# Kernel optimization log

Measured on AMD Instinct MI355X. Metric: run time of the kernel, lower is better.

## Reference

```python
import jax, jax.numpy as jnp
import numpy as np
from jax import lax

B, KLEN, KDIM, QDIM, ADIM, VDIM = 32, 2000, 512, 512, 512, 512
CONV_CH, CONV_K = 10, 201

def setup_inputs() -> dict:
    key = jax.random.key(0)
    ks = jax.random.split(key, 16)
    s = lambda fan: 1.0 / np.sqrt(fan)
    return {
        "key": jax.random.normal(ks[0], (B, KLEN, KDIM), jnp.float32),
        "value": jax.random.normal(ks[1], (B, KLEN, VDIM), jnp.float32),
        "query": jax.random.normal(ks[2], (B, 1, QDIM), jnp.float32),
        "aw_prev": jnp.zeros((B, 1, KLEN), jnp.float32),
        "mask": jnp.ones((B, 1, KLEN), jnp.int32),
        # parameters (torch nn.Linear: y = x @ W.T + b, W is [out,in])
        "Wk": jax.random.uniform(ks[3], (ADIM, KDIM), jnp.float32, -s(KDIM), s(KDIM)),
        "bk": jax.random.uniform(ks[4], (ADIM,), jnp.float32, -s(KDIM), s(KDIM)),
        "Wq": jax.random.uniform(ks[5], (ADIM, QDIM), jnp.float32, -s(QDIM), s(QDIM)),
        "conv_w": jax.random.uniform(ks[6], (CONV_CH, 1, CONV_K), jnp.float32, -s(CONV_K), s(CONV_K)),
        "Wconv": jax.random.uniform(ks[7], (ADIM, CONV_CH), jnp.float32, -s(CONV_CH), s(CONV_CH)),
        "v": jax.random.uniform(ks[8], (ADIM,), jnp.float32, -s(ADIM), s(ADIM)),
    }

def reference(key, value, query, aw_prev, mask, Wk, bk, Wq, conv_w, Wconv, v):
    # location-aware attention, qlen == 1, sharpening_factor == 1, no dropout (eval)
    kproj = jnp.einsum('bkd,ad->bka', key, Wk) + bk              # [B, klen, adim]
    qproj = jnp.einsum('bqd,ad->bqa', query, Wq)                 # [B, 1, adim]
    # conv over previous attention weights: 1D 'same' conv, 1 -> CONV_CH channels
    conv_feat = lax.conv_general_dilated(
        aw_prev, conv_w, window_strides=(1,), padding='SAME',
        dimension_numbers=('NCH', 'OIH', 'NCH'))                 # [B, C, klen]
    conv_proj = jnp.einsum('bck,ac->bka', conv_feat, Wconv)      # [B, klen, adim]
    # additive score: v^T tanh(Wk k + Wq q + Wc f)
    tmp = jnp.tanh(kproj[:, None] + qproj[:, :, None] + conv_proj[:, None])  # [B,1,klen,adim]
    e = jnp.einsum('bqka,a->bqk', tmp, v)                        # [B, 1, klen]
    neg_inf = jnp.finfo(e.dtype).min
    e = jnp.where(mask == 0, neg_inf, e)
    aw = jax.nn.softmax(e, axis=-1)                              # [B, 1, klen]
    cv = jnp.einsum('bqk,bkv->bqv', aw, value)                   # [B, 1, vdim]
    return cv, aw[:, None]  # aw: [B, 1(H), 1(qlen), klen]
```

## Files before the change

kernel.cpp:

```cpp
#include <hip/hip_runtime.h>
#include <hip/hip_bf16.h>
#include <math.h>

#define B 32
#define KLEN 2000
#define KDIM 512
#define QDIM 512
#define ADIM 512
#define VDIM 512
#define CONV_CH 10
#define CONV_K 201
#define NROWS (B*KLEN)

#define NKS  33
#define ZERO16 {0,0,0,0,0,0,0,0,0,0,0,0,0,0,0,0}

#define NP_PACK 53
#define NP_QPRJ 26
#define NP_CONV 256

typedef __attribute__((ext_vector_type(8)))  short bf16x8;
typedef __attribute__((ext_vector_type(16))) float f32x16;
typedef __attribute__((ext_vector_type(4)))  float f32x4;
typedef __attribute__((ext_vector_type(2)))  float f32x2;

__device__ __forceinline__ ushort f32_to_bf16(float f) {
    union { float f; unsigned int u; } v; v.f = f;
    unsigned int x = v.u;
    unsigned int r = (x + 0x7FFFu + ((x >> 16) & 1u)) >> 16;
    return (ushort)r;
}

__device__ __forceinline__ float fast_tanh(float x) {
    return 1.0f - 2.0f / (__expf(2.0f * x) + 1.0f);
}

#define MFMA32(a, bfr, c) __builtin_amdgcn_mfma_f32_32x32x16_bf16(a, bfr, c, 0, 0, 0)

__global__ __launch_bounds__(640, 2)
void k_prep(const float* __restrict__ Wk, const float* __restrict__ Wconv,
            const float* __restrict__ bk, ushort* __restrict__ wp,
            const float* __restrict__ query, const float* __restrict__ Wq,
            float* __restrict__ qproj,
            const float* __restrict__ aw_prev, const float* __restrict__ conv_w,
            float* __restrict__ cf) {
    __shared__ float w_s[CONV_CH * 204];
    __shared__ float aw_s[464];
    const int bid = blockIdx.x, tid = threadIdx.x;

    if (bid < NP_PACK) {
        int t = bid * 640 + tid;
        if (t < 16 * NKS * 64) {
            int lane = t & 63;
            int idx = t >> 6;
            int ks = idx % NKS, nt = idx / NKS;
            int h = lane >> 5, r = lane & 31;
            int a = nt * 32 + r;
            int j0 = ks * 16 + h * 8;
            union { uint4 v; ushort u[8]; } pk;
            #pragma unroll
            for (int jj = 0; jj < 8; jj++) {
                int j = j0 + jj;
                float val;
                if (j < 512)       val = Wk[a * KDIM + j];
                else if (j < 522)  val = Wconv[a * CONV_CH + (j - 512)];
                else if (j == 522) val = bk[a];
                else               val = 0.f;
                pk.u[jj] = f32_to_bf16(val);
            }
            *(uint4*)(wp + (size_t)t * 8) = pk.v;
        }
    } else if (bid < NP_PACK + NP_QPRJ) {
        int t = (bid - NP_PACK) * 640 + tid;
        if (t < B * ADIM) {
            int b = t >> 9, a = t & 511;
            const f32x4* q = (const f32x4*)(query + b * QDIM);
            const f32x4* w = (const f32x4*)(Wq + a * QDIM);
            float acc = 0.f;
            #pragma unroll 4
            for (int i = 0; i < 128; i++) {
                f32x4 qv = q[i], wv = w[i];
                acc += qv[0]*wv[0] + qv[1]*wv[1] + qv[2]*wv[2] + qv[3]*wv[3];
            }
            qproj[t] = acc;
        }
    } else {
        int cb = bid - NP_PACK - NP_QPRJ;
        int b = cb >> 3, chunk = cb & 7;
        int k0 = chunk * 256;
        for (int i = tid; i < CONV_CH * 204; i += 640) {
            int c = i / 204, t = i % 204;
            w_s[i] = (t < CONV_K) ? conv_w[c * CONV_K + t] : 0.f;
        }
        for (int i = tid; i < 464; i += 640) {
            int src = k0 - 100 + i;
            aw_s[i] = (src >= 0 && src < KLEN) ? aw_prev[b * KLEN + src] : 0.f;
        }
        __syncthreads();

        const int c = tid >> 6;
        const int k_local = (tid & 63) * 4;
        const float* wc = w_s + c * 204;
        float a0 = 0.f, a1 = 0.f, a2 = 0.f, a3 = 0.f;
        f32x4 r0 = *(const f32x4*)(aw_s + k_local);
        #pragma unroll 3
        for (int q = 0; q < 51; q++) {
            f32x4 r1 = *(const f32x4*)(aw_s + k_local + 4 * q + 4);
            float w0 = wc[4*q], w1 = wc[4*q+1], w2 = wc[4*q+2], w3 = wc[4*q+3];
            a0 += w0*r0[0]; a1 += w0*r0[1]; a2 += w0*r0[2]; a3 += w0*r0[3];
            a0 += w1*r0[1]; a1 += w1*r0[2]; a2 += w1*r0[3]; a3 += w1*r1[0];
            a0 += w2*r0[2]; a1 += w2*r0[3]; a2 += w2*r1[0]; a3 += w2*r1[1];
            a0 += w3*r0[3]; a1 += w3*r1[0]; a2 += w3*r1[1]; a3 += w3*r1[2];
            r0 = r1;
        }
        int k = k0 + k_local;
        float* dst = cf + ((size_t)b * CONV_CH + c) * KLEN + k;
        if (k + 3 < KLEN) {
            f32x4 o; o[0] = a0; o[1] = a1; o[2] = a2; o[3] = a3;
            *(f32x4*)dst = o;
        } else {
            if (k     < KLEN) dst[0] = a0;
            if (k + 1 < KLEN) dst[1] = a1;
            if (k + 2 < KLEN) dst[2] = a2;
            if (k + 3 < KLEN) dst[3] = a3;
        }
    }
}

__global__ __launch_bounds__(512, 4)
void k_main(const float* __restrict__ key, const ushort* __restrict__ wp,
            const float* __restrict__ qproj, const float* __restrict__ cf,
            const float* __restrict__ vvec, const int* __restrict__ mask,
            float* __restrict__ e_out) {
    __shared__ char Alds[65536];
    __shared__ float partsum[8][2][32];
    const int tid = threadIdx.x;
    const int wc = tid >> 6, lane = tid & 63;
    const int r = lane & 31, h = lane >> 5;
    const int b = blockIdx.x >> 5;
    const int kbase = (blockIdx.x & 31) * 64;

    #pragma unroll
    for (int i = 0; i < 8; i++) {
        int ch = tid + i * 512;
        int arow = ch >> 6, cx = ch & 63;
        int kpos = kbase + arow; if (kpos >= KLEN) kpos = KLEN - 1;
        const float* kp = key + ((size_t)b * KLEN + kpos) * KDIM + cx * 8;
        f32x4 f0 = __builtin_nontemporal_load((const f32x4*)kp);
        f32x4 f1 = __builtin_nontemporal_load((const f32x4*)(kp + 4));
        union { uint4 v; ushort u[8]; } pk;
        pk.u[0] = f32_to_bf16(f0[0]); pk.u[1] = f32_to_bf16(f0[1]);
        pk.u[2] = f32_to_bf16(f0[2]); pk.u[3] = f32_to_bf16(f0[3]);
        pk.u[4] = f32_to_bf16(f1[0]); pk.u[5] = f32_to_bf16(f1[1]);
        pk.u[6] = f32_to_bf16(f1[2]); pk.u[7] = f32_to_bf16(f1[3]);
        int off = arow * 1024 + cx * 16;
        off ^= (arow & 31) << 4;
        *(uint4*)(Alds + off) = pk.v;
    }
    __syncthreads();

    const ushort* bpW0 = wp + ((size_t)(wc * 2 + 0) * NKS * 64 + lane) * 8;
    const ushort* bpW1 = wp + ((size_t)(wc * 2 + 1) * NKS * 64 + lane) * 8;
    const int base_g0 = r * 1024 + h * 16;
    const int base_g1 = base_g0 + 32768;
    const int swz = r << 4;

    f32x16 c00 = ZERO16, c01 = ZERO16;
    f32x16 c10 = ZERO16, c11 = ZERO16;

    #pragma unroll 4
    for (int ks = 0; ks < 32; ks++) {
        bf16x8 k0 = *(const bf16x8*)(Alds + ((base_g0 + ks * 32) ^ swz));
        bf16x8 k1 = *(const bf16x8*)(Alds + ((base_g1 + ks * 32) ^ swz));
        bf16x8 w0 = *(const bf16x8*)(bpW0 + ks * 512);
        bf16x8 w1 = *(const bf16x8*)(bpW1 + ks * 512);
        c00 = MFMA32(w0, k0, c00); c01 = MFMA32(w0, k1, c01);
        c10 = MFMA32(w1, k0, c10); c11 = MFMA32(w1, k1, c11);
    }
    {
        auto build_ext = [&](int kpos) -> bf16x8 {
            int kc = kpos < KLEN ? kpos : KLEN - 1;
            const float* cfb = cf + ((size_t)b * CONV_CH) * KLEN + kc;
            union { bf16x8 v8; ushort u[8]; } pk;
            if (h == 0) {
                #pragma unroll
                for (int jj = 0; jj < 8; jj++) pk.u[jj] = f32_to_bf16(cfb[(size_t)jj * KLEN]);
            } else {
                pk.u[0] = f32_to_bf16(cfb[(size_t)8 * KLEN]);
                pk.u[1] = f32_to_bf16(cfb[(size_t)9 * KLEN]);
                pk.u[2] = 0x3F80;
                pk.u[3] = 0; pk.u[4] = 0; pk.u[5] = 0; pk.u[6] = 0; pk.u[7] = 0;
            }
            return pk.v8;
        };
        bf16x8 x0 = build_ext(kbase + r);
        bf16x8 x1 = build_ext(kbase + 32 + r);
        bf16x8 w0 = *(const bf16x8*)(bpW0 + 32 * 512);
        bf16x8 w1 = *(const bf16x8*)(bpW1 + 32 * 512);
        c00 = MFMA32(w0, x0, c00); c01 = MFMA32(w0, x1, c01);
        c10 = MFMA32(w1, x0, c10); c11 = MFMA32(w1, x1, c11);
    }

    const float* qb = qproj + b * ADIM + wc * 64;
    const float* vb = vvec + wc * 64;
    float pg0 = 0.f, pg1 = 0.f;
    #pragma unroll
    for (int t = 0; t < 2; t++) {
        const f32x16 a0 = t ? c10 : c00;
        const f32x16 a1 = t ? c11 : c01;
        #pragma unroll
        for (int q = 0; q < 4; q++) {
            f32x4 qv = *(const f32x4*)(qb + t * 32 + 8 * q + 4 * h);
            f32x4 vv = *(const f32x4*)(vb + t * 32 + 8 * q + 4 * h);
            #pragma unroll
            for (int j = 0; j < 4; j++) {
                int i = 4 * q + j;
                pg0 += fast_tanh(a0[i] + qv[j]) * vv[j];
                pg1 += fast_tanh(a1[i] + qv[j]) * vv[j];
            }
        }
    }
    pg0 += __shfl_xor(pg0, 32);
    pg1 += __shfl_xor(pg1, 32);
    if (h == 0) { partsum[wc][0][r] = pg0; partsum[wc][1][r] = pg1; }
    __syncthreads();

    if (tid < 64) {
        int g = tid >> 5, rr = tid & 31;
        float s = 0.f;
        #pragma unroll
        for (int w = 0; w < 8; w++) s += partsum[w][g][rr];
        int kpos = kbase + g * 32 + rr;
        if (kpos < KLEN) {
            int idx = b * KLEN + kpos;
            e_out[idx] = mask[idx] ? s : -3.4028235e38f;
        }
    }
}

__global__ void k_softmax(const float* __restrict__ e, float* __restrict__ aw) {
    int b = blockIdx.x;
    const float* er = e + b * KLEN;
    __shared__ float redm[4], reds[4];
    int tid = threadIdx.x, lane = tid & 63, wv = tid >> 6;
    float m = -3.4028235e38f;
    for (int k = tid; k < KLEN; k += 256) m = fmaxf(m, er[k]);
    for (int o = 32; o; o >>= 1) m = fmaxf(m, __shfl_xor(m, o));
    if (lane == 0) redm[wv] = m;
    __syncthreads();
    m = fmaxf(fmaxf(redm[0], redm[1]), fmaxf(redm[2], redm[3]));
    float s = 0.f;
    for (int k = tid; k < KLEN; k += 256) s += __expf(er[k] - m);
    for (int o = 32; o; o >>= 1) s += __shfl_xor(s, o);
    if (lane == 0) reds[wv] = s;
    __syncthreads();
    s = reds[0] + reds[1] + reds[2] + reds[3];
    float inv = 1.0f / s;
    for (int k = tid; k < KLEN; k += 256) aw[b * KLEN + k] = __expf(er[k] - m) * inv;
}

__global__ __launch_bounds__(512, 2)
void k_cvpart(const float* __restrict__ aw, const float* __restrict__ value,
              float* __restrict__ part) {
    int b = blockIdx.x >> 4, chunk = blockIdx.x & 15;
    int k0 = chunk * 125;
    __shared__ float sa[128];
    __shared__ f32x4 red[3][128];
    int tid = threadIdx.x;
    if (tid < 125) sa[tid] = aw[b * KLEN + k0 + tid];
    __syncthreads();
    const int kh = tid >> 7;
    const int colt = tid & 127;
    const float* vp = value + ((size_t)b * KLEN + k0) * VDIM + colt * 4;
    f32x4 acc = {0.f, 0.f, 0.f, 0.f};
    for (int k = kh; k < 125; k += 4) {
        f32x4 vv = __builtin_nontemporal_load((const f32x4*)(vp + (size_t)k * VDIM));
        acc += vv * sa[k];
    }
    if (kh) red[kh - 1][colt] = acc;
    __syncthreads();
    if (kh == 0) {
        acc += red[0][colt] + red[1][colt] + red[2][colt];
        *(f32x4*)(part + ((b * 16 + chunk) * VDIM) + colt * 4) = acc;
    }
}

__global__ void k_cvreduce(const float* __restrict__ part, float* __restrict__ cv) {
    int t = blockIdx.x * 256 + threadIdx.x;
    int b = t >> 9, col = t & 511;
    float s = 0.f;
    #pragma unroll
    for (int c = 0; c < 16; c++) s += part[(b * 16 + c) * VDIM + col];
    cv[t] = s;
}

extern "C" void kernel_launch(void* const* d_in, const int* in_sizes, int n_in,
                              void* d_out, int out_size, void* d_ws, size_t ws_size,
                              hipStream_t stream) {
    const float* key     = (const float*)d_in[0];
    const float* value   = (const float*)d_in[1];
    const float* query   = (const float*)d_in[2];
    const float* aw_prev = (const float*)d_in[3];
    const int*   mask    = (const int*)d_in[4];
    const float* Wk      = (const float*)d_in[5];
    const float* bk      = (const float*)d_in[6];
    const float* Wq      = (const float*)d_in[7];
    const float* conv_w  = (const float*)d_in[8];
    const float* Wconv   = (const float*)d_in[9];
    const float* vvec    = (const float*)d_in[10];

    char* ws = (char*)d_ws;
    ushort* wp   = (ushort*)(ws + 0);
    float* qproj = (float*)(ws + 540672);
    float* cf    = (float*)(ws + 606208);
    float* e     = (float*)(ws + 3166208);
    float* part  = (float*)(ws + 3422208);

    float* cv = (float*)d_out;
    float* aw = (float*)d_out + B * VDIM;

    k_prep    <<<NP_PACK + NP_QPRJ + NP_CONV, 640, 0, stream>>>(
                  Wk, Wconv, bk, wp, query, Wq, qproj, aw_prev, conv_w, cf);
    k_main    <<<1024, 512, 0, stream>>>(key, wp, qproj, cf, vvec, mask, e);
    k_softmax <<<B,    256, 0, stream>>>(e, aw);
    k_cvpart  <<<B*16, 512, 0, stream>>>(aw, value, part);
    k_cvreduce<<<64,   256, 0, stream>>>(part, cv);
}
```

Before: 142.7 us.

## Fuse softmax normalization into context-vector kernel and reduce partials with atomics

The softmax kernel now only computes per-batch max and reciprocal sum. The value-weighting kernel recomputes the normalized weights from the raw scores, writes them out, and accumulates the context vector directly with atomic adds into an output that the prep kernel zeroes. This drops the separate reduction kernel and one pass writing and re-reading the weights, and doubles the number of chunks for more parallelism. In exchange it adds float atomics, making the summation order nondeterministic, and it drops the nontemporal hint on the value loads.

```diff
diff --git a/kernel.cpp b/kernel.cpp
--- a/kernel.cpp
+++ b/kernel.cpp
@@ -17,7 +17,11 @@
 
 #define NP_PACK 53
 #define NP_QPRJ 26
+#define NP_ZERO 26
 #define NP_CONV 256
+
+#define CH_LEN 63
+#define CH_N   32
 
 typedef __attribute__((ext_vector_type(8)))  short bf16x8;
 typedef __attribute__((ext_vector_type(16))) float f32x16;
@@ -43,7 +47,7 @@
             const float* __restrict__ query, const float* __restrict__ Wq,
             float* __restrict__ qproj,
             const float* __restrict__ aw_prev, const float* __restrict__ conv_w,
-            float* __restrict__ cf) {
+            float* __restrict__ cf, float* __restrict__ cv) {
     __shared__ float w_s[CONV_CH * 204];
     __shared__ float aw_s[464];
     const int bid = blockIdx.x, tid = threadIdx.x;
@@ -84,8 +88,11 @@
             }
             qproj[t] = acc;
         }
+    } else if (bid < NP_PACK + NP_QPRJ + NP_ZERO) {
+        int t = (bid - NP_PACK - NP_QPRJ) * 640 + tid;
+        if (t < B * VDIM) cv[t] = 0.f;
     } else {
-        int cb = bid - NP_PACK - NP_QPRJ;
+        int cb = bid - NP_PACK - NP_QPRJ - NP_ZERO;
         int b = cb >> 3, chunk = cb & 7;
         int k0 = chunk * 256;
         for (int i = tid; i < CONV_CH * 204; i += 640) {
@@ -238,7 +245,7 @@
     }
 }
 
-__global__ void k_softmax(const float* __restrict__ e, float* __restrict__ aw) {
+__global__ void k_stats(const float* __restrict__ e, float* __restrict__ stats) {
     int b = blockIdx.x;
     const float* er = e + b * KLEN;
     __shared__ float redm[4], reds[4];
@@ -254,44 +261,48 @@
     for (int o = 32; o; o >>= 1) s += __shfl_xor(s, o);
     if (lane == 0) reds[wv] = s;
     __syncthreads();
-    s = reds[0] + reds[1] + reds[2] + reds[3];
-    float inv = 1.0f / s;
-    for (int k = tid; k < KLEN; k += 256) aw[b * KLEN + k] = __expf(er[k] - m) * inv;
-}
-
-__global__ __launch_bounds__(512, 2)
-void k_cvpart(const float* __restrict__ aw, const float* __restrict__ value,
-              float* __restrict__ part) {
-    int b = blockIdx.x >> 4, chunk = blockIdx.x & 15;
-    int k0 = chunk * 125;
-    __shared__ float sa[128];
+    if (tid == 0) {
+        s = reds[0] + reds[1] + reds[2] + reds[3];
+        stats[b * 2] = m;
+        stats[b * 2 + 1] = 1.0f / s;
+    }
+}
+
+__global__ __launch_bounds__(512, 4)
+void k_cvpart(const float* __restrict__ e, const float* __restrict__ stats,
+              const float* __restrict__ value, float* __restrict__ aw,
+              float* __restrict__ cv) {
+    int b = blockIdx.x >> 5, chunk = blockIdx.x & 31;
+    int k0 = chunk * CH_LEN;
+    int len = KLEN - k0; if (len > CH_LEN) len = CH_LEN;
+    __shared__ float sa[CH_LEN + 1];
     __shared__ f32x4 red[3][128];
     int tid = threadIdx.x;
-    if (tid < 125) sa[tid] = aw[b * KLEN + k0 + tid];
+    if (tid < len) {
+        float m = stats[b * 2], inv = stats[b * 2 + 1];
+        float p = __expf(e[b * KLEN + k0 + tid] - m) * inv;
+        sa[tid] = p;
+        aw[b * KLEN + k0 + tid] = p;
+    }
     __syncthreads();
     const int kh = tid >> 7;
     const int colt = tid & 127;
     const float* vp = value + ((size_t)b * KLEN + k0) * VDIM + colt * 4;
     f32x4 acc = {0.f, 0.f, 0.f, 0.f};
-    for (int k = kh; k < 125; k += 4) {
-        f32x4 vv = __builtin_nontemporal_load((const f32x4*)(vp + (size_t)k * VDIM));
+    for (int k = kh; k < len; k += 4) {
+        f32x4 vv = *(const f32x4*)(vp + (size_t)k * VDIM);
         acc += vv * sa[k];
     }
     if (kh) red[kh - 1][colt] = acc;
     __syncthreads();
     if (kh == 0) {
         acc += red[0][colt] + red[1][colt] + red[2][colt];
-        *(f32x4*)(part + ((b * 16 + chunk) * VDIM) + colt * 4) = acc;
-    }
-}
-
-__global__ void k_cvreduce(const float* __restrict__ part, float* __restrict__ cv) {
-    int t = blockIdx.x * 256 + threadIdx.x;
-    int b = t >> 9, col = t & 511;
-    float s = 0.f;
-    #pragma unroll
-    for (int c = 0; c < 16; c++) s += part[(b * 16 + c) * VDIM + col];
-    cv[t] = s;
+        float* dst = cv + b * VDIM + colt * 4;
+        atomicAdd(dst + 0, acc[0]);
+        atomicAdd(dst + 1, acc[1]);
+        atomicAdd(dst + 2, acc[2]);
+        atomicAdd(dst + 3, acc[3]);
+    }
 }
 
 extern "C" void kernel_launch(void* const* d_in, const int* in_sizes, int n_in,
@@ -314,15 +325,14 @@
     float* qproj = (float*)(ws + 540672);
     float* cf    = (float*)(ws + 606208);
     float* e     = (float*)(ws + 3166208);
-    float* part  = (float*)(ws + 3422208);
+    float* stats = (float*)(ws + 3422208);
 
     float* cv = (float*)d_out;
     float* aw = (float*)d_out + B * VDIM;
 
-    k_prep    <<<NP_PACK + NP_QPRJ + NP_CONV, 640, 0, stream>>>(
-                  Wk, Wconv, bk, wp, query, Wq, qproj, aw_prev, conv_w, cf);
-    k_main    <<<1024, 512, 0, stream>>>(key, wp, qproj, cf, vvec, mask, e);
-    k_softmax <<<B,    256, 0, stream>>>(e, aw);
-    k_cvpart  <<<B*16, 512, 0, stream>>>(aw, value, part);
-    k_cvreduce<<<64,   256, 0, stream>>>(part, cv);
-}
+    k_prep  <<<NP_PACK + NP_QPRJ + NP_ZERO + NP_CONV, 640, 0, stream>>>(
+                Wk, Wconv, bk, wp, query, Wq, qproj, aw_prev, conv_w, cf, cv);
+    k_main  <<<1024, 512, 0, stream>>>(key, wp, qproj, cf, vvec, mask, e);
+    k_stats <<<B,    256, 0, stream>>>(e, stats);
+    k_cvpart<<<B*32, 512, 0, stream>>>(e, stats, value, aw, cv);
+}
```

Result: no change. 141.8 us (-0.6%).
